# Kernel tuning notes

Measured on AMD Instinct MI355X. Metric: run time of the kernel, lower is better.

Reference implementation:

```python
import jax, jax.numpy as jnp
import numpy as np

M, N, D, L, DEPTH, WIDTH, BATCH = 64, 4096, 64, 32, 4, 256, 1024
WIN = 2 * L + 1


def setup_inputs() -> dict:
    key = jax.random.key(0)
    ks = jax.random.split(key, 5)
    u = jax.random.normal(ks[0], (BATCH, D), dtype=jnp.float32)
    # xavier-style scaled gaussians for weights, zeros for biases (matches torch init pattern)
    weight0 = jax.random.normal(ks[1], (M, WIDTH, D), dtype=jnp.float32) * (2.0 / (WIDTH + D)) ** 0.5
    bias0 = jnp.zeros((M, WIDTH, 1), dtype=jnp.float32)
    weight = jax.random.normal(ks[2], (DEPTH - 1, M, WIDTH, WIDTH), dtype=jnp.float32) * (1.0 / WIDTH) ** 0.5
    bias = jnp.zeros((DEPTH - 1, M, WIDTH, 1), dtype=jnp.float32)
    weight_final = jax.random.normal(ks[3], (M, WIN, WIDTH), dtype=jnp.float32) * (2.0 / (WIN + WIDTH)) ** 0.5
    bias_final = jnp.zeros((M, WIN, 1), dtype=jnp.float32)
    xi = jax.random.normal(ks[4], (M, N + 2 * L), dtype=jnp.float32) * (2.0 / (M + N + 2 * L)) ** 0.5
    return {"u": u, "weight0": weight0, "bias0": bias0, "weight": weight,
            "bias": bias, "weight_final": weight_final, "bias_final": bias_final, "xi": xi}


def reference(u, weight0, bias0, weight, bias, weight_final, bias_final, xi) -> jnp.ndarray:
    act = jax.nn.sigmoid
    # per-M shared MLP: u1 [M, width, batch]
    u1 = act(jnp.einsum('mwd,bd->mwb', weight0, u) + bias0)
    for i in range(weight.shape[0]):  # small fixed depth loop
        u1 = act(jnp.einsum('mwv,mvb->mwb', weight[i], u1) + bias[i])
    G = act(jnp.einsum('mjw,mwb->mjb', weight_final, u1) + bias_final)
    # sliding-window correlation: out[n, b] = sum_{m,j} xi[m, n+j] * G[m, j, b]
    win = G.shape[1]
    n_out = xi.shape[1] - (win - 1)
    idx = jnp.arange(n_out)[:, None] + jnp.arange(win)[None, :]
    xw = xi[:, idx]
    return jnp.einsum('mnj,mjb->nb', xw, G)  # [N, batch]
```

## Files before the change

### kernel.cpp

```cpp
#include <hip/hip_runtime.h>
#include <math.h>

typedef __attribute__((ext_vector_type(8))) short short8;
typedef __attribute__((ext_vector_type(4))) float floatx4;
typedef __attribute__((ext_vector_type(4))) unsigned short ushort4v;

__device__ __forceinline__ void load_lds16(const void* g, void* l) {
    __builtin_amdgcn_global_load_lds((const __attribute__((address_space(1))) void*)g,
                                     (__attribute__((address_space(3))) void*)l,
                                     16, 0, 0);
}

__device__ __forceinline__ unsigned short f2bf(float x) {
    union { float f; unsigned int u; } v; v.f = x;
    unsigned int r = v.u + 0x7fffu + ((v.u >> 16) & 1u);
    return (unsigned short)(r >> 16);
}

__device__ __forceinline__ float sigm(float x) { return 1.0f / (1.0f + __expf(-x)); }

__global__ void prep(const float* __restrict__ w0, const float* __restrict__ w,
                     const float* __restrict__ wf, const float* __restrict__ xi,
                     unsigned short* __restrict__ w0d, unsigned short* __restrict__ wd,
                     unsigned short* __restrict__ wfd, unsigned int* __restrict__ xw) {
    const int bid = blockIdx.x;
    if (bid < 6656) {
        const bool is0 = bid < 512;
        const int c = (is0 ? bid : bid - 512) * 256 + threadIdx.x;
        const int cpm = is0 ? 2048 : 8192;
        const int Kk  = is0 ? 2 : 8;
        const int K   = Kk * 32;
        const int mm  = c / cpm;
        const int cm  = c - mm * cpm;
        const int rblk = cm >> 6 >= 0 ? (cm / (Kk * 64)) : 0;
        const int rem  = cm - rblk * (Kk * 64);
        const int kk   = rem >> 6;
        const int lane = rem & 63;
        const int r  = rblk * 16 + (lane & 15);
        const int k0 = kk * 32 + (lane >> 4) * 8;
        const float* srcp = (is0 ? w0 : w) + ((size_t)mm * 256 + r) * K + k0;
        unsigned short* dstp = (is0 ? w0d : wd) + (size_t)c * 8;
        float4 a = *(const float4*)srcp;
        float4 b = *(const float4*)(srcp + 4);
        short8 o = { (short)f2bf(a.x), (short)f2bf(a.y), (short)f2bf(a.z), (short)f2bf(a.w),
                     (short)f2bf(b.x), (short)f2bf(b.y), (short)f2bf(b.z), (short)f2bf(b.w) };
        *(short8*)dstp = o;
    } else if (bid < 7680) {
        const int c = (bid - 6656) * 256 + threadIdx.x;
        const int m  = c >> 12;
        const int cm = c & 4095;
        const int rblk = cm >> 9;
        const int rem  = cm & 511;
        const int kk   = rem >> 6;
        const int lane = rem & 63;
        const int r  = rblk * 16 + (lane & 15);
        const int k0 = kk * 32 + (lane >> 4) * 8;
        short8 o = {0,0,0,0,0,0,0,0};
        if (r < 65) {
            const float* srcp = wf + ((size_t)m * 65 + r) * 256 + k0;
            float4 a = *(const float4*)srcp;
            float4 b = *(const float4*)(srcp + 4);
            o = (short8){ (short)f2bf(a.x), (short)f2bf(a.y), (short)f2bf(a.z), (short)f2bf(a.w),
                          (short)f2bf(b.x), (short)f2bf(b.y), (short)f2bf(b.z), (short)f2bf(b.w) };
        }
        *(short8*)(wfd + (size_t)c * 8) = o;
    } else {
        const int n = bid - 7680;
        #pragma unroll
        for (int t = 0; t < 9; ++t) {
            const int idx = t * 256 + threadIdx.x;
            if (idx < 2176) {
                const int m = idx / 34;
                const int pos = idx - m * 34;
                const int j0 = pos * 2;
                const float* xim = xi + (size_t)m * 4160 + n;
                const float v0 = (j0 < 65) ? xim[j0] : 0.0f;
                const float v1 = (j0 + 1 < 65) ? xim[j0 + 1] : 0.0f;
                xw[(size_t)n * 2176 + idx] =
                    (unsigned int)f2bf(v0) | ((unsigned int)f2bf(v1) << 16);
            }
        }
    }
}

template<int K, int I>
__device__ __forceinline__ void mlp_mfma(
    const unsigned short* __restrict__ Wt, const unsigned short* src,
    int wave, int lane, floatx4 (*acc)[4])
{
    const int Kk = K / 32;
    const int quad = lane >> 4, l16 = lane & 15;
    const int rblk0 = wave * I;
    const floatx4 zero = {0.f, 0.f, 0.f, 0.f};
    #pragma unroll
    for (int i = 0; i < I; ++i)
        #pragma unroll
        for (int j = 0; j < 4; ++j) acc[i][j] = zero;

    short8 af[I];
    #pragma unroll
    for (int i = 0; i < I; ++i)
        af[i] = *(const short8*)&Wt[(size_t)(((rblk0 + i) * Kk + 0) * 64 + lane) * 8];

    #pragma unroll
    for (int kk = 0; kk < Kk; ++kk) {
        short8 afn[I];
        if (kk + 1 < Kk) {
            #pragma unroll
            for (int i = 0; i < I; ++i)
                afn[i] = *(const short8*)&Wt[(size_t)(((rblk0 + i) * Kk + kk + 1) * 64 + lane) * 8];
        }
        short8 bf[4];
        #pragma unroll
        for (int j = 0; j < 4; ++j) {
            const int cb = j * 16 + l16;
            bf[j] = *(const short8*)&src[cb * K + (((kk * 4 + quad) ^ (cb & 7)) * 8)];
        }
        #pragma unroll
        for (int i = 0; i < I; ++i)
            #pragma unroll
            for (int j = 0; j < 4; ++j)
                acc[i][j] = __builtin_amdgcn_mfma_f32_16x16x32_bf16(af[i], bf[j], acc[i][j], 0, 0, 0);
        #pragma unroll
        for (int i = 0; i < I; ++i) af[i] = afn[i];
    }
}

__device__ __forceinline__ void mlp_write(
    const float* __restrict__ bm, unsigned short* dst,
    int wave, int lane, floatx4 (*acc)[4])
{
    const int quad = lane >> 4, l16 = lane & 15;
    const int rbw = wave * 64;
    #pragma unroll
    for (int i = 0; i < 4; ++i) {
        const int rb = rbw + i * 16 + quad * 4;
        float bv0 = bm[rb], bv1 = bm[rb + 1], bv2 = bm[rb + 2], bv3 = bm[rb + 3];
        #pragma unroll
        for (int j = 0; j < 4; ++j) {
            const int cb = j * 16 + l16;
            ushort4v o;
            o[0] = f2bf(sigm(acc[i][j][0] + bv0));
            o[1] = f2bf(sigm(acc[i][j][1] + bv1));
            o[2] = f2bf(sigm(acc[i][j][2] + bv2));
            o[3] = f2bf(sigm(acc[i][j][3] + bv3));
            *(ushort4v*)&dst[cb * 256 + (((rb >> 3) ^ (cb & 7)) * 8) + (rb & 7)] = o;
        }
    }
}

__global__ __launch_bounds__(256, 2)
void fused_mlp(const float* __restrict__ u,
               const unsigned short* __restrict__ w0_bf, const float* __restrict__ b0_,
               const unsigned short* __restrict__ w_bf,  const float* __restrict__ b_,
               const unsigned short* __restrict__ wf_bf, const float* __restrict__ bf_,
               unsigned short* __restrict__ Gflat) {
    __shared__ unsigned short X[64 * 256];

    const int bid = blockIdx.x;
    const int xcd = bid & 7, slot = bid >> 3;
    const int m  = (xcd << 3) + (slot >> 4);
    const int b0 = (slot & 15) << 6;
    const int tid = threadIdx.x, wave = tid >> 6, lane = tid & 63;

    {
        const int b = tid >> 2, dc = tid & 3;
        const float* up = u + (size_t)(b0 + b) * 64 + dc * 16;
        float4 v0 = *(const float4*)(up);
        float4 v1 = *(const float4*)(up + 4);
        float4 v2 = *(const float4*)(up + 8);
        float4 v3 = *(const float4*)(up + 12);
        short8 c0 = { (short)f2bf(v0.x), (short)f2bf(v0.y), (short)f2bf(v0.z), (short)f2bf(v0.w),
                      (short)f2bf(v1.x), (short)f2bf(v1.y), (short)f2bf(v1.z), (short)f2bf(v1.w) };
        short8 c1 = { (short)f2bf(v2.x), (short)f2bf(v2.y), (short)f2bf(v2.z), (short)f2bf(v2.w),
                      (short)f2bf(v3.x), (short)f2bf(v3.y), (short)f2bf(v3.z), (short)f2bf(v3.w) };
        *(short8*)&X[b * 64 + (((dc * 2)     ^ (b & 7)) * 8)] = c0;
        *(short8*)&X[b * 64 + (((dc * 2 + 1) ^ (b & 7)) * 8)] = c1;
    }
    __syncthreads();

    floatx4 acc[4][4];

    mlp_mfma<64, 4>(w0_bf + (size_t)m * 16384, X, wave, lane, acc);
    __syncthreads();
    mlp_write(b0_ + (size_t)m * 256, X, wave, lane, acc);
    __syncthreads();

    #pragma unroll 1
    for (int l = 0; l < 3; ++l) {
        mlp_mfma<256, 4>(w_bf + ((size_t)l * 64 + m) * 65536, X, wave, lane, acc);
        __syncthreads();
        mlp_write(b_ + ((size_t)l * 64 + m) * 256, X, wave, lane, acc);
        __syncthreads();
    }

    {
        floatx4 acf[2][4];
        mlp_mfma<256, 2>(wf_bf + (size_t)m * 32768, X, wave, lane, acf);
        const int quad = lane >> 4, l16 = lane & 15;
        const float* bm = bf_ + (size_t)m * 65;
        unsigned short* Gg = Gflat + (size_t)b0 * 4352 + m * 68;
        #pragma unroll
        for (int i = 0; i < 2; ++i) {
            const int rb = wave * 32 + i * 16 + quad * 4;
            if (rb < 68) {
                float bv[4];
                #pragma unroll
                for (int rr = 0; rr < 4; ++rr)
                    bv[rr] = (rb + rr < 65) ? bm[rb + rr] : 0.0f;
                #pragma unroll
                for (int j = 0; j < 4; ++j) {
                    const int cb = j * 16 + l16;
                    ushort4v o;
                    #pragma unroll
                    for (int rr = 0; rr < 4; ++rr)
                        o[rr] = f2bf(sigm(acf[i][j][rr] + bv[rr]));
                    *(ushort4v*)&Gg[(size_t)cb * 4352 + rb] = o;
                }
            }
        }
    }
}

__global__ __launch_bounds__(256, 3)
void contract_gemm(const unsigned short* __restrict__ XW,
                   const unsigned short* __restrict__ G,
                   float* __restrict__ P) {
    const int bid = blockIdx.x;
    const int xcd = bid & 7, slot = bid >> 3;
    const int kc  = slot >> 5;
    const int rst = slot & 31;
    const int r0 = ((xcd << 2) + (rst >> 3)) << 7;
    const int c0 = (rst & 7) << 7;
    const int kb = kc * 1088;
    float* Pc = P + (size_t)kc * 4096 * 1024;

    __shared__ unsigned short As[128 * 64];
    __shared__ unsigned short Bs[128 * 64];

    const int tid = threadIdx.x;
    const int wave = tid >> 6, lane = tid & 63;
    const int quad = lane >> 4, l16 = lane & 15;
    const int wr = (wave & 1) * 64;
    const int wc = (wave >> 1) * 64;
    const int srow = wave * 32 + (lane >> 3);
    const int spos = lane & 7;

    floatx4 acc[4][4];
    const floatx4 zero = {0.f, 0.f, 0.f, 0.f};
    #pragma unroll
    for (int i = 0; i < 4; ++i)
        #pragma unroll
        for (int j = 0; j < 4; ++j) acc[i][j] = zero;

    for (int k0 = kb; k0 < kb + 1088; k0 += 64) {
        #pragma unroll
        for (int t = 0; t < 4; ++t) {
            const int row = srow + t * 8;
            const int fc  = spos ^ (row & 7);
            load_lds16(XW + (size_t)(r0 + row) * 4352 + k0 + fc * 8,
                       &As[(wave * 32 + t * 8) * 64]);
            load_lds16(G + (size_t)(c0 + row) * 4352 + k0 + fc * 8,
                       &Bs[(wave * 32 + t * 8) * 64]);
        }
        __syncthreads();

        #pragma unroll
        for (int kk = 0; kk < 2; ++kk) {
            short8 af[4], bfr[4];
            #pragma unroll
            for (int i = 0; i < 4; ++i) {
                const int ra = wr + i * 16 + l16;
                af[i]  = *(const short8*)&As[ra * 64 + (((kk * 4 + quad) ^ (ra & 7)) * 8)];
                const int cb = wc + i * 16 + l16;
                bfr[i] = *(const short8*)&Bs[cb * 64 + (((kk * 4 + quad) ^ (cb & 7)) * 8)];
            }
            #pragma unroll
            for (int i = 0; i < 4; ++i)
                #pragma unroll
                for (int j = 0; j < 4; ++j)
                    acc[i][j] = __builtin_amdgcn_mfma_f32_16x16x32_bf16(af[i], bfr[j], acc[i][j], 0, 0, 0);
        }
        __syncthreads();
    }

    #pragma unroll
    for (int i = 0; i < 4; ++i) {
        const int rb = r0 + wr + i * 16 + quad * 4;
        #pragma unroll
        for (int rr = 0; rr < 4; ++rr)
            #pragma unroll
            for (int j = 0; j < 4; ++j) {
                const int col = c0 + wc + j * 16 + l16;
                Pc[(size_t)(rb + rr) * 1024 + col] = acc[i][j][rr];
            }
    }
}

__global__ void reduce4(const float* __restrict__ P, float* __restrict__ out) {
    const int i = blockIdx.x * 256 + threadIdx.x;
    const float4* p = (const float4*)P;
    float4 a = p[i], b = p[i + 1048576], c = p[i + 2097152], d = p[i + 3145728];
    ((float4*)out)[i] = (float4){ a.x + b.x + c.x + d.x, a.y + b.y + c.y + d.y,
                                  a.z + b.z + c.z + d.z, a.w + b.w + c.w + d.w };
}

extern "C" void kernel_launch(void* const* d_in, const int* in_sizes, int n_in,
                              void* d_out, int out_size, void* d_ws, size_t ws_size,
                              hipStream_t stream) {
    const float* u   = (const float*)d_in[0];
    const float* w0  = (const float*)d_in[1];
    const float* b0_ = (const float*)d_in[2];
    const float* w   = (const float*)d_in[3];
    const float* b   = (const float*)d_in[4];
    const float* wf  = (const float*)d_in[5];
    const float* bf_ = (const float*)d_in[6];
    const float* xi  = (const float*)d_in[7];
    float* out = (float*)d_out;

    unsigned short* w0_bf = (unsigned short*)d_ws;
    unsigned short* w_bf  = w0_bf + 1048576;
    unsigned short* wf_bf = w_bf  + 12582912;
    unsigned short* Gflat = wf_bf + 2097152;
    unsigned short* XW    = Gflat + 4456448;
    float*          P     = (float*)(XW + 17825792);

    prep<<<11776, 256, 0, stream>>>(w0, w, wf, xi, w0_bf, w_bf, wf_bf, (unsigned int*)XW);
    fused_mlp<<<1024, 256, 0, stream>>>(u, w0_bf, b0_, w_bf, b, wf_bf, bf_, Gflat);
    contract_gemm<<<1024, 256, 0, stream>>>(XW, Gflat, P);
    reduce4<<<4096, 256, 0, stream>>>(P, out);
}
```

Baseline: 262.6 us.

## Cut MLP kernel register pressure and cheapen sigmoid epilogue for higher occupancy

Drops the register double-buffering of weight fragments in the MFMA loop and raises the fused_mlp launch bound from 2 to 3 blocks per SIMD. This trades software prefetch of weight fragments for more resident waves to hide latency. It also rewrites the sigmoid epilogue to use exp2 and reciprocal intrinsics with the bias folded into an FMA, and packs bf16 pairs with a byte-permute. That packing rounds half-up instead of round-to-nearest-even, a small numerical change.

```diff
diff --git a/kernel.cpp b/kernel.cpp
--- a/kernel.cpp
+++ b/kernel.cpp
@@ -16,6 +16,30 @@
     unsigned int r = v.u + 0x7fffu + ((v.u >> 16) & 1u);
     return (unsigned short)(r >> 16);
 }
+
+__device__ __forceinline__ unsigned int pack_bf(float f0, float f1) {
+    union { float f; unsigned int u; } a, b;
+    a.f = f0; b.f = f1;
+    return __builtin_amdgcn_perm(b.u + 0x8000u, a.u + 0x8000u, 0x07060302u);
+}
+
+__device__ __forceinline__ float fast_exp2(float x) {
+#if __has_builtin(__builtin_amdgcn_exp2f)
+    return __builtin_amdgcn_exp2f(x);
+#else
+    return __expf(x * 0.69314718056f);
+#endif
+}
+
+__device__ __forceinline__ float fast_rcp(float x) {
+#if __has_builtin(__builtin_amdgcn_rcpf)
+    return __builtin_amdgcn_rcpf(x);
+#else
+    return 1.0f / x;
+#endif
+}
+
+#define NEG_LOG2E (-1.4426950408889634f)
 
 __device__ __forceinline__ float sigm(float x) { return 1.0f / (1.0f + __expf(-x)); }
 
@@ -32,7 +56,7 @@
         const int K   = Kk * 32;
         const int mm  = c / cpm;
         const int cm  = c - mm * cpm;
-        const int rblk = cm >> 6 >= 0 ? (cm / (Kk * 64)) : 0;
+        const int rblk = cm / (Kk * 64);
         const int rem  = cm - rblk * (Kk * 64);
         const int kk   = rem >> 6;
         const int lane = rem & 63;
@@ -97,20 +121,12 @@
         #pragma unroll
         for (int j = 0; j < 4; ++j) acc[i][j] = zero;
 
-    short8 af[I];
-    #pragma unroll
-    for (int i = 0; i < I; ++i)
-        af[i] = *(const short8*)&Wt[(size_t)(((rblk0 + i) * Kk + 0) * 64 + lane) * 8];
-
     #pragma unroll
     for (int kk = 0; kk < Kk; ++kk) {
-        short8 afn[I];
-        if (kk + 1 < Kk) {
-            #pragma unroll
-            for (int i = 0; i < I; ++i)
-                afn[i] = *(const short8*)&Wt[(size_t)(((rblk0 + i) * Kk + kk + 1) * 64 + lane) * 8];
-        }
-        short8 bf[4];
+        short8 af[I], bf[4];
+        #pragma unroll
+        for (int i = 0; i < I; ++i)
+            af[i] = *(const short8*)&Wt[(size_t)(((rblk0 + i) * Kk + kk) * 64 + lane) * 8];
         #pragma unroll
         for (int j = 0; j < 4; ++j) {
             const int cb = j * 16 + l16;
@@ -121,8 +137,6 @@
             #pragma unroll
             for (int j = 0; j < 4; ++j)
                 acc[i][j] = __builtin_amdgcn_mfma_f32_16x16x32_bf16(af[i], bf[j], acc[i][j], 0, 0, 0);
-        #pragma unroll
-        for (int i = 0; i < I; ++i) af[i] = afn[i];
     }
 }
 
@@ -135,21 +149,24 @@
     #pragma unroll
     for (int i = 0; i < 4; ++i) {
         const int rb = rbw + i * 16 + quad * 4;
-        float bv0 = bm[rb], bv1 = bm[rb + 1], bv2 = bm[rb + 2], bv3 = bm[rb + 3];
+        float c0 = bm[rb]     * NEG_LOG2E;
+        float c1 = bm[rb + 1] * NEG_LOG2E;
+        float c2 = bm[rb + 2] * NEG_LOG2E;
+        float c3 = bm[rb + 3] * NEG_LOG2E;
         #pragma unroll
         for (int j = 0; j < 4; ++j) {
             const int cb = j * 16 + l16;
-            ushort4v o;
-            o[0] = f2bf(sigm(acc[i][j][0] + bv0));
-            o[1] = f2bf(sigm(acc[i][j][1] + bv1));
-            o[2] = f2bf(sigm(acc[i][j][2] + bv2));
-            o[3] = f2bf(sigm(acc[i][j][3] + bv3));
-            *(ushort4v*)&dst[cb * 256 + (((rb >> 3) ^ (cb & 7)) * 8) + (rb & 7)] = o;
-        }
-    }
-}
-
-__global__ __launch_bounds__(256, 2)
+            float r0 = fast_rcp(1.0f + fast_exp2(fmaf(acc[i][j][0], NEG_LOG2E, c0)));
+            float r1 = fast_rcp(1.0f + fast_exp2(fmaf(acc[i][j][1], NEG_LOG2E, c1)));
+            float r2 = fast_rcp(1.0f + fast_exp2(fmaf(acc[i][j][2], NEG_LOG2E, c2)));
+            float r3 = fast_rcp(1.0f + fast_exp2(fmaf(acc[i][j][3], NEG_LOG2E, c3)));
+            uint2 o = { pack_bf(r0, r1), pack_bf(r2, r3) };
+            *(uint2*)&dst[cb * 256 + (((rb >> 3) ^ (cb & 7)) * 8) + (rb & 7)] = o;
+        }
+    }
+}
+
+__global__ __launch_bounds__(256, 3)
 void fused_mlp(const float* __restrict__ u,
                const unsigned short* __restrict__ w0_bf, const float* __restrict__ b0_,
                const unsigned short* __restrict__ w_bf,  const float* __restrict__ b_,
@@ -170,12 +187,12 @@
         float4 v1 = *(const float4*)(up + 4);
         float4 v2 = *(const float4*)(up + 8);
         float4 v3 = *(const float4*)(up + 12);
-        short8 c0 = { (short)f2bf(v0.x), (short)f2bf(v0.y), (short)f2bf(v0.z), (short)f2bf(v0.w),
-                      (short)f2bf(v1.x), (short)f2bf(v1.y), (short)f2bf(v1.z), (short)f2bf(v1.w) };
-        short8 c1 = { (short)f2bf(v2.x), (short)f2bf(v2.y), (short)f2bf(v2.z), (short)f2bf(v2.w),
-                      (short)f2bf(v3.x), (short)f2bf(v3.y), (short)f2bf(v3.z), (short)f2bf(v3.w) };
-        *(short8*)&X[b * 64 + (((dc * 2)     ^ (b & 7)) * 8)] = c0;
-        *(short8*)&X[b * 64 + (((dc * 2 + 1) ^ (b & 7)) * 8)] = c1;
+        uint4 p0 = { pack_bf(v0.x, v0.y), pack_bf(v0.z, v0.w),
+                     pack_bf(v1.x, v1.y), pack_bf(v1.z, v1.w) };
+        uint4 p1 = { pack_bf(v2.x, v2.y), pack_bf(v2.z, v2.w),
+                     pack_bf(v3.x, v3.y), pack_bf(v3.z, v3.w) };
+        *(uint4*)&X[b * 64 + (((dc * 2)     ^ (b & 7)) * 8)] = p0;
+        *(uint4*)&X[b * 64 + (((dc * 2 + 1) ^ (b & 7)) * 8)] = p1;
     }
     __syncthreads();
 
@@ -204,18 +221,19 @@
         for (int i = 0; i < 2; ++i) {
             const int rb = wave * 32 + i * 16 + quad * 4;
             if (rb < 68) {
-                float bv[4];
+                float c[4];
                 #pragma unroll
                 for (int rr = 0; rr < 4; ++rr)
-                    bv[rr] = (rb + rr < 65) ? bm[rb + rr] : 0.0f;
+                    c[rr] = (rb + rr < 65) ? bm[rb + rr] * NEG_LOG2E : 0.0f;
                 #pragma unroll
                 for (int j = 0; j < 4; ++j) {
                     const int cb = j * 16 + l16;
-                    ushort4v o;
-                    #pragma unroll
-                    for (int rr = 0; rr < 4; ++rr)
-                        o[rr] = f2bf(sigm(acf[i][j][rr] + bv[rr]));
-                    *(ushort4v*)&Gg[(size_t)cb * 4352 + rb] = o;
+                    float r0 = fast_rcp(1.0f + fast_exp2(fmaf(acf[i][j][0], NEG_LOG2E, c[0])));
+                    float r1 = fast_rcp(1.0f + fast_exp2(fmaf(acf[i][j][1], NEG_LOG2E, c[1])));
+                    float r2 = fast_rcp(1.0f + fast_exp2(fmaf(acf[i][j][2], NEG_LOG2E, c[2])));
+                    float r3 = fast_rcp(1.0f + fast_exp2(fmaf(acf[i][j][3], NEG_LOG2E, c[3])));
+                    uint2 o = { pack_bf(r0, r1), pack_bf(r2, r3) };
+                    *(uint2*)&Gg[(size_t)cb * 4352 + rb] = o;
                 }
             }
         }
```

Result: faster. 230.0 us (-12.4%).
